# Kernel tuning notes

Measured on AMD Instinct MI355X. Metric: run time of the kernel, lower is better.

## Reference

```python
import jax, jax.numpy as jnp
import numpy as np

B, T, D, I, E, R = 4, 2048, 2048, 6144, 8, 32


def setup_inputs() -> dict:
    key = jax.random.key(0)
    ks = jax.random.split(key, 9)
    return {
        "x": jax.random.normal(ks[0], (B, T, D), jnp.float32),
        "router_w": jax.random.normal(ks[1], (D, E), jnp.float32) * 0.02,
        "A_gate": jax.random.normal(ks[2], (E, D, R), jnp.float32) * 0.01,
        "B_gate": jax.random.normal(ks[3], (E, R, I), jnp.float32) * 0.01,
        "A_up": jax.random.normal(ks[4], (E, D, R), jnp.float32) * 0.01,
        "B_up": jax.random.normal(ks[5], (E, R, I), jnp.float32) * 0.01,
        "W_gate": jax.random.normal(ks[6], (D, I), jnp.float32) * 0.02,
        "W_up": jax.random.normal(ks[7], (D, I), jnp.float32) * 0.02,
        "W_down": jax.random.normal(ks[8], (I, D), jnp.float32) * 0.02,
    }


def reference(x, router_w, A_gate, B_gate, A_up, B_up, W_gate, W_up, W_down):
    b, t, d = x.shape
    flat = x.reshape(b * t, d)                     # [N, D]
    # Router: top-1 expert per token (argmax matches torch argmax: first max)
    gate_logits = flat @ router_w                  # [N, E]
    idx = jnp.argmax(gate_logits, axis=-1)         # [N]
    n_exp = router_w.shape[1]

    def routed_lora(A, Bm):
        # sum_e mask_e * (x @ A_e @ B_e); loop over small static expert count
        out = jnp.zeros((flat.shape[0], Bm.shape[2]), flat.dtype)
        for e in range(n_exp):
            m = (idx == e)[:, None]
            out = out + jnp.where(m, (flat @ A[e]) @ Bm[e], 0.0)
        return out

    # ExpertLoRA forward: base gate/up + per-token-selected LoRA delta, SwiGLU, down
    gate = flat @ W_gate + routed_lora(A_gate, B_gate)   # [N, I]
    up = flat @ W_up + routed_lora(A_up, B_up)           # [N, I]
    down = (jax.nn.silu(gate) * up) @ W_down             # [N, D]
    return down.reshape(b, t, d), gate_logits
```

## Files before the change

kernel.cpp:

```cpp
#include <hip/hip_runtime.h>
#include <stdint.h>

#define N_TOK 8192
#define DDIM 2048
#define IDIM 6144
#define NEXP 8
#define RLORA 32
#define NCHUNK 64
#define CHUNK 128

typedef __attribute__((ext_vector_type(8))) short short8;
typedef __attribute__((ext_vector_type(4))) float floatx4;
typedef __attribute__((ext_vector_type(4))) unsigned short ushortx4;

__device__ __forceinline__ unsigned short f2bf(float f) {
  union { float f; unsigned u; } v; v.f = f;
  unsigned u = v.u;
  unsigned r = (u + 0x7fffu + ((u >> 16) & 1u)) >> 16;
  return (unsigned short)r;
}

__device__ __forceinline__ void gload_lds16(const void* g, void* l) {
  __builtin_amdgcn_global_load_lds(
      (const __attribute__((address_space(1))) void*)g,
      (__attribute__((address_space(3))) void*)l, 16, 0, 0);
}

__global__ __launch_bounds__(256) void router_kernel(
    const float* __restrict__ x, const float* __restrict__ rw,
    float* __restrict__ logits_out, int* __restrict__ idx) {
  int wave = threadIdx.x >> 6, lane = threadIdx.x & 63;
  int n = blockIdx.x * 4 + wave;
  const float* xr = x + (size_t)n * DDIM;
  float acc[NEXP];
#pragma unroll
  for (int e = 0; e < NEXP; e++) acc[e] = 0.f;
#pragma unroll
  for (int j = 0; j < 8; j++) {
    int d = j * 256 + lane * 4;
    floatx4 v = *(const floatx4*)(xr + d);
    const float* rwd = rw + (size_t)d * NEXP;
#pragma unroll
    for (int t = 0; t < 4; t++) {
      float xv = v[t];
      const float* rr = rwd + t * NEXP;
#pragma unroll
      for (int e = 0; e < NEXP; e++) acc[e] += xv * rr[e];
    }
  }
#pragma unroll
  for (int off = 32; off > 0; off >>= 1) {
#pragma unroll
    for (int e = 0; e < NEXP; e++) acc[e] += __shfl_xor(acc[e], off, 64);
  }
  if (lane == 0) {
    float best = acc[0]; int bi = 0;
#pragma unroll
    for (int e = 1; e < NEXP; e++)
      if (acc[e] > best) { best = acc[e]; bi = e; }
    idx[n] = bi;
#pragma unroll
    for (int e = 0; e < NEXP; e++) logits_out[(size_t)n * NEXP + e] = acc[e];
  }
}

__global__ __launch_bounds__(128) void count_kernel(
    const int* __restrict__ idx, int* __restrict__ cnt) {
  __shared__ int h[NEXP];
  if (threadIdx.x < NEXP) h[threadIdx.x] = 0;
  __syncthreads();
  int n = blockIdx.x * CHUNK + threadIdx.x;
  atomicAdd(&h[idx[n]], 1);
  __syncthreads();
  if (threadIdx.x < NEXP) cnt[blockIdx.x * NEXP + threadIdx.x] = h[threadIdx.x];
}

__global__ __launch_bounds__(64) void scan_kernel(
    const int* __restrict__ cnt, int* __restrict__ off) {
  __shared__ int tot[NEXP], base[NEXP];
  int t = threadIdx.x;
  if (t < NEXP) {
    int s = 0;
    for (int c = 0; c < NCHUNK; c++) s += cnt[c * NEXP + t];
    tot[t] = s;
  }
  __syncthreads();
  if (t == 0) {
    int run = 0;
    for (int e = 0; e < NEXP; e++) { base[e] = run; run += tot[e]; }
  }
  __syncthreads();
  if (t < NEXP) {
    int run = base[t];
    for (int c = 0; c < NCHUNK; c++) { off[c * NEXP + t] = run; run += cnt[c * NEXP + t]; }
  }
}

__global__ __launch_bounds__(64) void rank_kernel(
    const int* __restrict__ idx, const int* __restrict__ off,
    int* __restrict__ sortpos, int* __restrict__ orig, int* __restrict__ eidx) {
  if (threadIdx.x != 0) return;
  int c = blockIdx.x;
  int lc[NEXP];
#pragma unroll
  for (int e = 0; e < NEXP; e++) lc[e] = 0;
  for (int t = 0; t < CHUNK; t++) {
    int n = c * CHUNK + t;
    int e = idx[n];
    int dst = off[c * NEXP + e] + lc[e]++;
    sortpos[n] = dst;
    orig[dst] = n;
    eidx[dst] = e;
  }
}

__global__ __launch_bounds__(256) void permute_x_kernel(
    const float* __restrict__ x, const int* __restrict__ sortpos,
    unsigned short* __restrict__ xb) {
  int wave = threadIdx.x >> 6, lane = threadIdx.x & 63;
  int n = blockIdx.x * 4 + wave;
  int dst = sortpos[n];
  const float* xr = x + (size_t)n * DDIM;
  unsigned short* xbr = xb + (size_t)dst * DDIM;
#pragma unroll
  for (int j = 0; j < 8; j++) {
    int d = j * 256 + lane * 4;
    floatx4 v = *(const floatx4*)(xr + d);
    ushortx4 s;
    s[0] = f2bf(v[0]); s[1] = f2bf(v[1]); s[2] = f2bf(v[2]); s[3] = f2bf(v[3]);
    *(ushortx4*)(xbr + d) = s;
  }
}

__global__ __launch_bounds__(256) void transpose_w_kernel(
    const float* __restrict__ in, unsigned short* __restrict__ out, int Rr, int Cc) {
  __shared__ float lds[32][33];
  int r0 = blockIdx.y * 32, c0 = blockIdx.x * 32;
  int tx = threadIdx.x & 31, ty = threadIdx.x >> 5;
#pragma unroll
  for (int k = 0; k < 4; k++) {
    int r = ty + k * 8;
    lds[r][tx] = in[(size_t)(r0 + r) * Cc + c0 + tx];
  }
  __syncthreads();
#pragma unroll
  for (int k = 0; k < 4; k++) {
    int cc = ty + k * 8;
    out[(size_t)(c0 + cc) * Rr + r0 + tx] = f2bf(lds[tx][cc]);
  }
}

__global__ __launch_bounds__(256) void transpose_wint_kernel(
    const float* __restrict__ Wg, const float* __restrict__ Wu,
    unsigned short* __restrict__ wint) {
  __shared__ float lds[32][33];
  int r0 = blockIdx.y * 32, c0 = blockIdx.x * 32;
  const float* in = blockIdx.z ? Wu : Wg;
  int w = blockIdx.z;
  int tx = threadIdx.x & 31, ty = threadIdx.x >> 5;
#pragma unroll
  for (int k = 0; k < 4; k++) {
    int r = ty + k * 8;
    lds[r][tx] = in[(size_t)(r0 + r) * IDIM + c0 + tx];
  }
  __syncthreads();
#pragma unroll
  for (int k = 0; k < 4; k++) {
    int cc = ty + k * 8;
    wint[(size_t)(2 * (c0 + cc) + w) * DDIM + r0 + tx] = f2bf(lds[tx][cc]);
  }
}

__global__ __launch_bounds__(256) void pack_a_kernel(
    const float* __restrict__ Ag, const float* __restrict__ Au,
    unsigned short* __restrict__ aat) {
  int o = blockIdx.x * 256 + threadIdx.x;
  int h = o >> 19;
  int oo = o & ((1 << 19) - 1);
  int c = oo >> 11, d = oo & 2047;
  int e = c >> 5, r = c & 31;
  const float* src = h ? Au : Ag;
  float v = src[(e << 16) + (d << 5) + r];
  aat[(size_t)(h * 256 + c) * DDIM + d] = f2bf(v);
}

__global__ __launch_bounds__(256) void pack_bl_kernel(
    const float* __restrict__ Bg, const float* __restrict__ Bu,
    unsigned short* __restrict__ BL) {
  int o = (blockIdx.x * 256 + threadIdx.x) * 4;
  int kk = o & 63;
  int t2 = o >> 6;
  int c = t2 % (2 * IDIM);
  int e = t2 / (2 * IDIM);
  int j = c >> 1, w = c & 1;
  ushortx4 s;
#pragma unroll
  for (int r = 0; r < 4; r++) {
    int k = kk + r;
    float v;
    if (w == 0) v = (k < 32) ? Bg[((size_t)e * RLORA + k) * IDIM + j] : 0.f;
    else        v = (k >= 32) ? Bu[((size_t)e * RLORA + (k - 32)) * IDIM + j] : 0.f;
    s[r] = f2bf(v);
  }
  *(ushortx4*)(BL + o) = s;
}

__global__ __launch_bounds__(256) void gemm_tsel_kernel(
    const unsigned short* __restrict__ xb, const unsigned short* __restrict__ aat,
    const int* __restrict__ eidx, unsigned short* __restrict__ Tsel) {
  __shared__ __align__(16) unsigned short sA[4096], sB[2048];
  __shared__ int es_s[128];
  const int row0 = blockIdx.x * 128;
  const int tid = threadIdx.x;
  const int wave = tid >> 6, lane = tid & 63;
  const int wr = wave >> 1, wc = wave & 1;
  const int q = lane >> 4, m16 = lane & 15;
  if (tid < 128) es_s[tid] = eidx[row0 + tid];
  __syncthreads();
  const int emin = es_s[0], emax = es_s[127];
  int erow[4];
#pragma unroll
  for (int m = 0; m < 4; m++) erow[m] = es_s[wr * 64 + m * 16 + m16];
  floatx4 acc[8];
#pragma unroll
  for (int i = 0; i < 8; i++)
#pragma unroll
    for (int j = 0; j < 4; j++) acc[i][j] = 0.f;
  short8 zero;
#pragma unroll
  for (int i = 0; i < 8; i++) zero[i] = 0;
  for (int ee = emin; ee <= emax; ee++) {
    for (int k0 = 0; k0 < DDIM; k0 += 32) {
      __syncthreads();
#pragma unroll
      for (int rr = 0; rr < 2; rr++) {
        int e = tid * 8 + rr * 2048;
        int r = e >> 5, kk = e & 31;
        gload_lds16(xb + (size_t)(row0 + r) * DDIM + (k0 + kk), sA + e);
      }
      {
        int e2 = tid * 8;
        int c = e2 >> 5, kk = e2 & 31;
        int srow = (c < 32) ? (ee * 32 + c) : (256 + ee * 32 + (c - 32));
        gload_lds16(aat + (size_t)srow * DDIM + (k0 + kk), sB + e2);
      }
      __syncthreads();
      short8 a[4], b[2];
#pragma unroll
      for (int m = 0; m < 4; m++) {
        short8 av = *(const short8*)(sA + (wr * 64 + m * 16 + m16) * 32 + q * 8);
        a[m] = (erow[m] == ee) ? av : zero;
      }
#pragma unroll
      for (int n = 0; n < 2; n++)
        b[n] = *(const short8*)(sB + (wc * 32 + n * 16 + m16) * 32 + q * 8);
#pragma unroll
      for (int m = 0; m < 4; m++)
#pragma unroll
        for (int n = 0; n < 2; n++)
          acc[m * 2 + n] = __builtin_amdgcn_mfma_f32_16x16x32_bf16(a[m], b[n], acc[m * 2 + n], 0, 0, 0);
    }
  }
#pragma unroll
  for (int m = 0; m < 4; m++)
#pragma unroll
    for (int n = 0; n < 2; n++)
#pragma unroll
      for (int r = 0; r < 4; r++) {
        int grow = row0 + wr * 64 + m * 16 + q * 4 + r;
        int gcol = wc * 32 + n * 16 + m16;
        Tsel[(size_t)grow * 64 + gcol] = f2bf(acc[m * 2 + n][r]);
      }
}

__global__ __launch_bounds__(512, 2) void gemm_gateup_kernel(
    const unsigned short* __restrict__ xb, const unsigned short* __restrict__ wint,
    const unsigned short* __restrict__ Tsel, const unsigned short* __restrict__ BL,
    const int* __restrict__ eidx, unsigned short* __restrict__ hbuf) {
  __shared__ __align__(16) unsigned short smem[65536];

  int lin = blockIdx.x;
  int xcd = lin & 7, slot = lin >> 3;
  int grp = slot >> 6, r = slot & 63;
  int bx = xcd * 6 + grp * 2 + (r & 1);
  int by = r >> 1;
  const int row0 = by * 256, col0 = bx * 256;

  const int tid = threadIdx.x;
  const int lane = tid & 63, wave = tid >> 6;
  const int wm = wave >> 2, wn = wave & 3;
  const int q = lane >> 4, m16 = lane & 15;

  floatx4 acc[32];
#pragma unroll
  for (int i = 0; i < 32; i++)
#pragma unroll
    for (int j = 0; j < 4; j++) acc[i][j] = 0.f;

  auto stage = [&](int kt) {
    unsigned short* Ab = smem + (kt & 3) * 16384;
    unsigned short* Bb = Ab + 8192;
#pragma unroll
    for (int ch = 0; ch < 2; ch++) {
      int o = ch * 4096 + tid * 8;
      int rw2 = o >> 5, g = (o >> 3) & 3;
      int gs = g ^ ((rw2 >> 1) & 3);
      gload_lds16(xb + (size_t)(row0 + rw2) * DDIM + kt * 32 + gs * 8, Ab + o);
    }
#pragma unroll
    for (int ch = 0; ch < 2; ch++) {
      int o = ch * 4096 + tid * 8;
      int rw2 = o >> 5, g = (o >> 3) & 3;
      int gs = g ^ ((rw2 >> 1) & 3);
      gload_lds16(wint + (size_t)(col0 + rw2) * DDIM + kt * 32 + gs * 8, Bb + o);
    }
  };

  stage(0); stage(1); stage(2);

  int offA[8], offB[4];
#pragma unroll
  for (int m = 0; m < 8; m++) {
    int rw2 = wm * 128 + m * 16 + m16;
    offA[m] = rw2 * 32 + ((q ^ ((rw2 >> 1) & 3)) * 8);
  }
#pragma unroll
  for (int n = 0; n < 4; n++) {
    int c = wn * 64 + n * 16 + m16;
    offB[n] = 8192 + c * 32 + ((q ^ ((c >> 1) & 3)) * 8);
  }

  for (int kt = 0; kt < 64; kt++) {
    if (kt < 62)      asm volatile("s_waitcnt vmcnt(8)" ::: "memory");
    else if (kt == 62) asm volatile("s_waitcnt vmcnt(4)" ::: "memory");
    else               asm volatile("s_waitcnt vmcnt(0)" ::: "memory");
    __builtin_amdgcn_s_barrier();
    __builtin_amdgcn_sched_barrier(0);
    if (kt + 3 < 64) stage(kt + 3);
    const unsigned short* base = smem + (kt & 3) * 16384;
    short8 a[8], b[4];
#pragma unroll
    for (int m = 0; m < 8; m++) a[m] = *(const short8*)(base + offA[m]);
#pragma unroll
    for (int n = 0; n < 4; n++) b[n] = *(const short8*)(base + offB[n]);
    __builtin_amdgcn_s_setprio(1);
#pragma unroll
    for (int m = 0; m < 8; m++)
#pragma unroll
      for (int n = 0; n < 4; n++)
        acc[m * 4 + n] = __builtin_amdgcn_mfma_f32_16x16x32_bf16(a[m], b[n], acc[m * 4 + n], 0, 0, 0);
    __builtin_amdgcn_s_setprio(0);
  }

#pragma unroll
  for (int ch = 0; ch < 4; ch++) {
    int o = ch * 4096 + tid * 8;
    int rw2 = o >> 6, g = (o >> 3) & 7;
    int gs = g ^ (rw2 & 7);
    gload_lds16(Tsel + (size_t)(row0 + rw2) * 64 + gs * 8, smem + o);
  }
  int* es = (int*)(smem + 32768);
  if (tid < 64) gload_lds16(eidx + row0 + tid * 4, (void*)(es + tid * 4));
  asm volatile("s_waitcnt vmcnt(0)" ::: "memory");
  __builtin_amdgcn_s_barrier();
  __builtin_amdgcn_sched_barrier(0);

  const int emin = es[0], emax = es[255];
  int erow[8];
#pragma unroll
  for (int m = 0; m < 8; m++) erow[m] = es[wm * 128 + m * 16 + m16];

  auto stage_bl = [&](int ee) {
#pragma unroll
    for (int ch = 0; ch < 4; ch++) {
      int o = ch * 4096 + tid * 8;
      int c = o >> 6, g = (o >> 3) & 7;
      int gs = g ^ (c & 7);
      gload_lds16(BL + ((size_t)ee * (2 * IDIM) + col0 + c) * 64 + gs * 8, smem + 16384 + o);
    }
  };
  stage_bl(emin);
  asm volatile("s_waitcnt vmcnt(0)" ::: "memory");
  __builtin_amdgcn_s_barrier();
  __builtin_amdgcn_sched_barrier(0);

  short8 zero;
#pragma unroll
  for (int i = 0; i < 8; i++) zero[i] = 0;

  for (int ee = emin; ee <= emax; ee++) {
    short8 bl[4][2];
#pragma unroll
    for (int n = 0; n < 4; n++) {
      int c = wn * 64 + n * 16 + m16;
#pragma unroll
      for (int kk = 0; kk < 2; kk++) {
        int gg = (kk * 4 + q) ^ (c & 7);
        bl[n][kk] = *(const short8*)(smem + 16384 + c * 64 + gg * 8);
      }
    }
#pragma unroll
    for (int m = 0; m < 8; m++) {
      int rw2 = wm * 128 + m * 16 + m16;
      short8 tgm[2];
#pragma unroll
      for (int kk = 0; kk < 2; kk++) {
        int gg = (kk * 4 + q) ^ (rw2 & 7);
        short8 v = *(const short8*)(smem + rw2 * 64 + gg * 8);
        tgm[kk] = (erow[m] == ee) ? v : zero;
      }
#pragma unroll
      for (int n = 0; n < 4; n++)
#pragma unroll
        for (int kk = 0; kk < 2; kk++)
          acc[m * 4 + n] = __builtin_amdgcn_mfma_f32_16x16x32_bf16(tgm[kk], bl[n][kk], acc[m * 4 + n], 0, 0, 0);
    }
    if (ee < emax) {
      __builtin_amdgcn_s_barrier();
      stage_bl(ee + 1);
      asm volatile("s_waitcnt vmcnt(0)" ::: "memory");
      __builtin_amdgcn_s_barrier();
      __builtin_amdgcn_sched_barrier(0);
    }
  }

#pragma unroll
  for (int m = 0; m < 8; m++)
#pragma unroll
    for (int n = 0; n < 4; n++)
#pragma unroll
      for (int rr2 = 0; rr2 < 4; rr2++) {
        float v = acc[m * 4 + n][rr2];
        float p = __shfl_xor(v, 1, 64);
        float g = (m16 & 1) ? p : v;
        float u = (m16 & 1) ? v : p;
        float h = g / (1.f + __expf(-g)) * u;
        if (!(m16 & 1)) {
          int grow = row0 + wm * 128 + m * 16 + q * 4 + rr2;
          int gi = (col0 + wn * 64 + n * 16 + m16) >> 1;
          hbuf[(size_t)grow * IDIM + gi] = f2bf(h);
        }
      }
}

__device__ __forceinline__ void mm_main(const unsigned short* __restrict__ Ab,
                                        const unsigned short* __restrict__ Bb,
                                        int K, int row0, int col0,
                                        unsigned short* sA, unsigned short* sB,
                                        floatx4* acc) {
  const int tid = threadIdx.x;
  const int wave = tid >> 6, lane = tid & 63;
  const int wr = wave >> 1, wc = wave & 1;
  const int q = lane >> 4, m16 = lane & 15;
  for (int k0 = 0; k0 < K; k0 += 32) {
    __syncthreads();
#pragma unroll
    for (int rr = 0; rr < 2; rr++) {
      int e = tid * 8 + rr * 2048;
      int r = e >> 5, kk = e & 31;
      gload_lds16(Ab + (size_t)(row0 + r) * K + (k0 + kk), sA + e);
      gload_lds16(Bb + (size_t)(col0 + r) * K + (k0 + kk), sB + e);
    }
    __syncthreads();
    short8 a[4], b[4];
#pragma unroll
    for (int m = 0; m < 4; m++)
      a[m] = *(const short8*)(sA + (wr * 64 + m * 16 + m16) * 32 + q * 8);
#pragma unroll
    for (int n = 0; n < 4; n++)
      b[n] = *(const short8*)(sB + (wc * 64 + n * 16 + m16) * 32 + q * 8);
#pragma unroll
    for (int m = 0; m < 4; m++)
#pragma unroll
      for (int n = 0; n < 4; n++)
        acc[m * 4 + n] = __builtin_amdgcn_mfma_f32_16x16x32_bf16(a[m], b[n], acc[m * 4 + n], 0, 0, 0);
  }
}

__global__ __launch_bounds__(256) void gemm_down_kernel(
    const unsigned short* __restrict__ hb, const unsigned short* __restrict__ wdt,
    const int* __restrict__ orig, float* __restrict__ out) {
  __shared__ __align__(16) unsigned short sA[4096], sB[4096];
  floatx4 acc[16];
#pragma unroll
  for (int i = 0; i < 16; i++)
#pragma unroll
    for (int j = 0; j < 4; j++) acc[i][j] = 0.f;
  int lin = blockIdx.x;
  int xcd = lin & 7, slot = lin >> 3;
  int bx = xcd * 2 + (slot & 1);
  int by = slot >> 1;
  int row0 = by * 128, col0 = bx * 128;
  mm_main(hb, wdt, IDIM, row0, col0, sA, sB, acc);
  const int wave = threadIdx.x >> 6, lane = threadIdx.x & 63;
  const int wr = wave >> 1, wc = wave & 1;
  const int q = lane >> 4, m16 = lane & 15;
#pragma unroll
  for (int m = 0; m < 4; m++)
#pragma unroll
    for (int n = 0; n < 4; n++)
#pragma unroll
      for (int r = 0; r < 4; r++) {
        int grow = row0 + wr * 64 + m * 16 + q * 4 + r;
        int orow = orig[grow];
        int gcol = col0 + wc * 64 + n * 16 + m16;
        out[(size_t)orow * DDIM + gcol] = acc[m * 4 + n][r];
      }
}

extern "C" void kernel_launch(void* const* d_in, const int* in_sizes, int n_in,
                              void* d_out, int out_size, void* d_ws, size_t ws_size,
                              hipStream_t stream) {
  const float* x  = (const float*)d_in[0];
  const float* rw = (const float*)d_in[1];
  const float* Ag = (const float*)d_in[2];
  const float* Bg = (const float*)d_in[3];
  const float* Au = (const float*)d_in[4];
  const float* Bu = (const float*)d_in[5];
  const float* Wg = (const float*)d_in[6];
  const float* Wu = (const float*)d_in[7];
  const float* Wd = (const float*)d_in[8];
  float* out = (float*)d_out;
  float* logits = out + (size_t)N_TOK * DDIM;

  char* ws = (char*)d_ws;
  size_t off = 0;
  auto alloc = [&](size_t bytes) {
    char* p = ws + off;
    off += (bytes + 255) & ~(size_t)255;
    return p;
  };
  unsigned short* xb  = (unsigned short*)alloc((size_t)N_TOK * DDIM * 2);
  unsigned short* wint= (unsigned short*)alloc((size_t)2 * IDIM * DDIM * 2);
  unsigned short* wdt = (unsigned short*)alloc((size_t)DDIM * IDIM * 2);
  unsigned short* aat = (unsigned short*)alloc((size_t)512 * DDIM * 2);
  unsigned short* BL  = (unsigned short*)alloc((size_t)NEXP * 2 * IDIM * 64 * 2);
  unsigned short* Tsel= (unsigned short*)alloc((size_t)N_TOK * 64 * 2);
  unsigned short* hbuf= (unsigned short*)alloc((size_t)N_TOK * IDIM * 2);
  int* idx     = (int*)alloc((size_t)N_TOK * 4);
  int* sortpos = (int*)alloc((size_t)N_TOK * 4);
  int* orig    = (int*)alloc((size_t)N_TOK * 4);
  int* eidx    = (int*)alloc((size_t)N_TOK * 4);
  int* cnt     = (int*)alloc((size_t)NCHUNK * NEXP * 4);
  int* offb    = (int*)alloc((size_t)NCHUNK * NEXP * 4);

  router_kernel<<<N_TOK / 4, 256, 0, stream>>>(x, rw, logits, idx);
  count_kernel<<<NCHUNK, 128, 0, stream>>>(idx, cnt);
  scan_kernel<<<1, 64, 0, stream>>>(cnt, offb);
  rank_kernel<<<NCHUNK, 64, 0, stream>>>(idx, offb, sortpos, orig, eidx);
  permute_x_kernel<<<N_TOK / 4, 256, 0, stream>>>(x, sortpos, xb);
  transpose_w_kernel<<<dim3(DDIM / 32, IDIM / 32), 256, 0, stream>>>(Wd, wdt, IDIM, DDIM);
  transpose_wint_kernel<<<dim3(IDIM / 32, DDIM / 32, 2), 256, 0, stream>>>(Wg, Wu, wint);
  pack_a_kernel<<<4096, 256, 0, stream>>>(Ag, Au, aat);
  pack_bl_kernel<<<(NEXP * 2 * IDIM * 64) / 1024, 256, 0, stream>>>(Bg, Bu, BL);
  gemm_tsel_kernel<<<N_TOK / 128, 256, 0, stream>>>(xb, aat, eidx, Tsel);
  gemm_gateup_kernel<<<(N_TOK / 256) * (2 * IDIM / 256), 512, 0, stream>>>(
      xb, wint, Tsel, BL, eidx, hbuf);
  gemm_down_kernel<<<(DDIM / 128) * (N_TOK / 128), 256, 0, stream>>>(hbuf, wdt, orig, out);
}
```

Measured before the change: 1.151 ms.

## Share a split-phase pipelined 256x256 GEMM mainloop between gate/up and down kernels

Factors the gate/up mainloop into a shared routine that splits each K step into two half-tiles of MFMAs, interleaving the A and B prefetch loads between them with extra barriers and priority hints. The down-projection GEMM moves from a simple single-buffered 128x128 tile loop to this 4-stage, swizzled, 256x256 tile routine with 512 threads. The aim is to hide global-to-LDS latency and LDS bank conflicts in the down GEMM and to overlap memory with MFMA work in both GEMMs. The cost is more barriers per K step and only 256 blocks in the down kernel, which may underfill the GPU.

New measurement: 1.058 ms. 8.1% less time.

```diff
diff --git a/kernel.cpp b/kernel.cpp
--- a/kernel.cpp
+++ b/kernel.cpp
@@ -273,6 +273,93 @@
       }
 }
 
+__device__ __forceinline__ void mm256_main(const unsigned short* __restrict__ Aptr,
+                                           const unsigned short* __restrict__ Bptr,
+                                           int K, int row0, int col0,
+                                           unsigned short* smem, floatx4* acc) {
+  const int tid = threadIdx.x;
+  const int lane = tid & 63, wave = tid >> 6;
+  const int wm = wave >> 2, wn = wave & 3;
+  const int q = lane >> 4, m16 = lane & 15;
+  const int NT = K >> 5;
+
+  int offA[8], offB[4];
+#pragma unroll
+  for (int m = 0; m < 8; m++) {
+    int rw2 = wm * 128 + m * 16 + m16;
+    offA[m] = rw2 * 32 + ((q ^ ((rw2 >> 1) & 3)) * 8);
+  }
+#pragma unroll
+  for (int n = 0; n < 4; n++) {
+    int c = wn * 64 + n * 16 + m16;
+    offB[n] = 8192 + c * 32 + ((q ^ ((c >> 1) & 3)) * 8);
+  }
+
+  auto stageA = [&](int kt) {
+    unsigned short* Ab = smem + (kt & 3) * 16384;
+#pragma unroll
+    for (int ch = 0; ch < 2; ch++) {
+      int o = ch * 4096 + tid * 8;
+      int rw2 = o >> 5, g = (o >> 3) & 3;
+      int gs = g ^ ((rw2 >> 1) & 3);
+      gload_lds16(Aptr + (size_t)(row0 + rw2) * K + kt * 32 + gs * 8, Ab + o);
+    }
+  };
+  auto stageB = [&](int kt) {
+    unsigned short* Bb = smem + (kt & 3) * 16384 + 8192;
+#pragma unroll
+    for (int ch = 0; ch < 2; ch++) {
+      int o = ch * 4096 + tid * 8;
+      int rw2 = o >> 5, g = (o >> 3) & 3;
+      int gs = g ^ ((rw2 >> 1) & 3);
+      gload_lds16(Bptr + (size_t)(col0 + rw2) * K + kt * 32 + gs * 8, Bb + o);
+    }
+  };
+
+  stageA(0); stageB(0); stageA(1); stageB(1); stageA(2); stageB(2);
+  asm volatile("s_waitcnt vmcnt(8)" ::: "memory");
+  __builtin_amdgcn_s_barrier();
+  __builtin_amdgcn_sched_barrier(0);
+
+  for (int kt = 0; kt < NT; kt++) {
+    const unsigned short* base = smem + (kt & 3) * 16384;
+    short8 a[4], b[4];
+#pragma unroll
+    for (int m = 0; m < 4; m++) a[m] = *(const short8*)(base + offA[m]);
+#pragma unroll
+    for (int n = 0; n < 4; n++) b[n] = *(const short8*)(base + offB[n]);
+    if (kt + 3 < NT) stageA(kt + 3);
+    __builtin_amdgcn_s_barrier();
+    asm volatile("s_waitcnt lgkmcnt(0)" ::: "memory");
+    __builtin_amdgcn_sched_barrier(0);
+    __builtin_amdgcn_s_setprio(1);
+#pragma unroll
+    for (int m = 0; m < 4; m++)
+#pragma unroll
+      for (int n = 0; n < 4; n++)
+        acc[m * 4 + n] = __builtin_amdgcn_mfma_f32_16x16x32_bf16(a[m], b[n], acc[m * 4 + n], 0, 0, 0);
+    __builtin_amdgcn_s_setprio(0);
+    __builtin_amdgcn_s_barrier();
+#pragma unroll
+    for (int m = 0; m < 4; m++) a[m] = *(const short8*)(base + offA[4 + m]);
+    if (kt + 3 < NT) stageB(kt + 3);
+    if (kt < NT - 3)       asm volatile("s_waitcnt vmcnt(8)" ::: "memory");
+    else if (kt == NT - 3) asm volatile("s_waitcnt vmcnt(4)" ::: "memory");
+    else if (kt == NT - 2) asm volatile("s_waitcnt vmcnt(0)" ::: "memory");
+    __builtin_amdgcn_s_barrier();
+    asm volatile("s_waitcnt lgkmcnt(0)" ::: "memory");
+    __builtin_amdgcn_sched_barrier(0);
+    __builtin_amdgcn_s_setprio(1);
+#pragma unroll
+    for (int m = 0; m < 4; m++)
+#pragma unroll
+      for (int n = 0; n < 4; n++)
+        acc[16 + m * 4 + n] = __builtin_amdgcn_mfma_f32_16x16x32_bf16(a[m], b[n], acc[16 + m * 4 + n], 0, 0, 0);
+    __builtin_amdgcn_s_setprio(0);
+    __builtin_amdgcn_s_barrier();
+  }
+}
+
 __global__ __launch_bounds__(512, 2) void gemm_gateup_kernel(
     const unsigned short* __restrict__ xb, const unsigned short* __restrict__ wint,
     const unsigned short* __restrict__ Tsel, const unsigned short* __restrict__ BL,
@@ -297,60 +384,7 @@
 #pragma unroll
     for (int j = 0; j < 4; j++) acc[i][j] = 0.f;
 
-  auto stage = [&](int kt) {
-    unsigned short* Ab = smem + (kt & 3) * 16384;
-    unsigned short* Bb = Ab + 8192;
-#pragma unroll
-    for (int ch = 0; ch < 2; ch++) {
-      int o = ch * 4096 + tid * 8;
-      int rw2 = o >> 5, g = (o >> 3) & 3;
-      int gs = g ^ ((rw2 >> 1) & 3);
-      gload_lds16(xb + (size_t)(row0 + rw2) * DDIM + kt * 32 + gs * 8, Ab + o);
-    }
-#pragma unroll
-    for (int ch = 0; ch < 2; ch++) {
-      int o = ch * 4096 + tid * 8;
-      int rw2 = o >> 5, g = (o >> 3) & 3;
-      int gs = g ^ ((rw2 >> 1) & 3);
-      gload_lds16(wint + (size_t)(col0 + rw2) * DDIM + kt * 32 + gs * 8, Bb + o);
-    }
-  };
-
-  stage(0); stage(1); stage(2);
-
-  int offA[8], offB[4];
-#pragma unroll
-  for (int m = 0; m < 8; m++) {
-    int rw2 = wm * 128 + m * 16 + m16;
-    offA[m] = rw2 * 32 + ((q ^ ((rw2 >> 1) & 3)) * 8);
-  }
-#pragma unroll
-  for (int n = 0; n < 4; n++) {
-    int c = wn * 64 + n * 16 + m16;
-    offB[n] = 8192 + c * 32 + ((q ^ ((c >> 1) & 3)) * 8);
-  }
-
-  for (int kt = 0; kt < 64; kt++) {
-    if (kt < 62)      asm volatile("s_waitcnt vmcnt(8)" ::: "memory");
-    else if (kt == 62) asm volatile("s_waitcnt vmcnt(4)" ::: "memory");
-    else               asm volatile("s_waitcnt vmcnt(0)" ::: "memory");
-    __builtin_amdgcn_s_barrier();
-    __builtin_amdgcn_sched_barrier(0);
-    if (kt + 3 < 64) stage(kt + 3);
-    const unsigned short* base = smem + (kt & 3) * 16384;
-    short8 a[8], b[4];
-#pragma unroll
-    for (int m = 0; m < 8; m++) a[m] = *(const short8*)(base + offA[m]);
-#pragma unroll
-    for (int n = 0; n < 4; n++) b[n] = *(const short8*)(base + offB[n]);
-    __builtin_amdgcn_s_setprio(1);
-#pragma unroll
-    for (int m = 0; m < 8; m++)
-#pragma unroll
-      for (int n = 0; n < 4; n++)
-        acc[m * 4 + n] = __builtin_amdgcn_mfma_f32_16x16x32_bf16(a[m], b[n], acc[m * 4 + n], 0, 0, 0);
-    __builtin_amdgcn_s_setprio(0);
-  }
+  mm256_main(xb, wint, DDIM, row0, col0, smem, acc);
 
 #pragma unroll
   for (int ch = 0; ch < 4; ch++) {
@@ -443,67 +477,35 @@
       }
 }
 
-__device__ __forceinline__ void mm_main(const unsigned short* __restrict__ Ab,
-                                        const unsigned short* __restrict__ Bb,
-                                        int K, int row0, int col0,
-                                        unsigned short* sA, unsigned short* sB,
-                                        floatx4* acc) {
-  const int tid = threadIdx.x;
-  const int wave = tid >> 6, lane = tid & 63;
-  const int wr = wave >> 1, wc = wave & 1;
-  const int q = lane >> 4, m16 = lane & 15;
-  for (int k0 = 0; k0 < K; k0 += 32) {
-    __syncthreads();
-#pragma unroll
-    for (int rr = 0; rr < 2; rr++) {
-      int e = tid * 8 + rr * 2048;
-      int r = e >> 5, kk = e & 31;
-      gload_lds16(Ab + (size_t)(row0 + r) * K + (k0 + kk), sA + e);
-      gload_lds16(Bb + (size_t)(col0 + r) * K + (k0 + kk), sB + e);
-    }
-    __syncthreads();
-    short8 a[4], b[4];
-#pragma unroll
-    for (int m = 0; m < 4; m++)
-      a[m] = *(const short8*)(sA + (wr * 64 + m * 16 + m16) * 32 + q * 8);
-#pragma unroll
-    for (int n = 0; n < 4; n++)
-      b[n] = *(const short8*)(sB + (wc * 64 + n * 16 + m16) * 32 + q * 8);
-#pragma unroll
-    for (int m = 0; m < 4; m++)
-#pragma unroll
-      for (int n = 0; n < 4; n++)
-        acc[m * 4 + n] = __builtin_amdgcn_mfma_f32_16x16x32_bf16(a[m], b[n], acc[m * 4 + n], 0, 0, 0);
-  }
-}
-
-__global__ __launch_bounds__(256) void gemm_down_kernel(
+__global__ __launch_bounds__(512, 2) void gemm_down_kernel(
     const unsigned short* __restrict__ hb, const unsigned short* __restrict__ wdt,
     const int* __restrict__ orig, float* __restrict__ out) {
-  __shared__ __align__(16) unsigned short sA[4096], sB[4096];
-  floatx4 acc[16];
-#pragma unroll
-  for (int i = 0; i < 16; i++)
+  __shared__ __align__(16) unsigned short smem[65536];
+  int lin = blockIdx.x;
+  int bx = lin & 7, by = lin >> 3;
+  const int row0 = by * 256, col0 = bx * 256;
+
+  floatx4 acc[32];
+#pragma unroll
+  for (int i = 0; i < 32; i++)
 #pragma unroll
     for (int j = 0; j < 4; j++) acc[i][j] = 0.f;
-  int lin = blockIdx.x;
-  int xcd = lin & 7, slot = lin >> 3;
-  int bx = xcd * 2 + (slot & 1);
-  int by = slot >> 1;
-  int row0 = by * 128, col0 = bx * 128;
-  mm_main(hb, wdt, IDIM, row0, col0, sA, sB, acc);
-  const int wave = threadIdx.x >> 6, lane = threadIdx.x & 63;
-  const int wr = wave >> 1, wc = wave & 1;
+
+  mm256_main(hb, wdt, IDIM, row0, col0, smem, acc);
+
+  const int tid = threadIdx.x;
+  const int lane = tid & 63, wave = tid >> 6;
+  const int wm = wave >> 2, wn = wave & 3;
   const int q = lane >> 4, m16 = lane & 15;
 #pragma unroll
-  for (int m = 0; m < 4; m++)
+  for (int m = 0; m < 8; m++)
 #pragma unroll
     for (int n = 0; n < 4; n++)
 #pragma unroll
       for (int r = 0; r < 4; r++) {
-        int grow = row0 + wr * 64 + m * 16 + q * 4 + r;
+        int grow = row0 + wm * 128 + m * 16 + q * 4 + r;
         int orow = orig[grow];
-        int gcol = col0 + wc * 64 + n * 16 + m16;
+        int gcol = col0 + wn * 64 + n * 16 + m16;
         out[(size_t)orow * DDIM + gcol] = acc[m * 4 + n][r];
       }
 }
@@ -556,5 +558,5 @@
   gemm_tsel_kernel<<<N_TOK / 128, 256, 0, stream>>>(xb, aat, eidx, Tsel);
   gemm_gateup_kernel<<<(N_TOK / 256) * (2 * IDIM / 256), 512, 0, stream>>>(
       xb, wint, Tsel, BL, eidx, hbuf);
-  gemm_down_kernel<<<(DDIM / 128) * (N_TOK / 128), 256, 0, stream>>>(hbuf, wdt, orig, out);
-}
+  gemm_down_kernel<<<256, 512, 0, stream>>>(hbuf, wdt, orig, out);
+}
```
